# Kernel optimization log

Measured on AMD Instinct MI355X. Metric: run time of the kernel, lower is better.

## Reference

```python
import jax, jax.numpy as jnp
import numpy as np

B, S, D, H = 2, 2048, 1024, 16
DK = D // H


def setup_inputs() -> dict:
    key = jax.random.key(0)
    ks = jax.random.split(key, 6)
    inp = {
        "mha_input": jax.random.normal(ks[0], (B, S, D), dtype=jnp.float32),
        "mask": jax.random.randint(ks[1], (B, S), 0, 2, dtype=jnp.int32),
        "Wq_w": jax.random.normal(ks[2], (D, D), dtype=jnp.float32) * 0.02,
        "Wq_b": jnp.zeros((D,), dtype=jnp.float32),
        "Wk_w": jax.random.normal(ks[3], (D, D), dtype=jnp.float32) * 0.02,
        "Wk_b": jnp.zeros((D,), dtype=jnp.float32),
        "Wv_w": jax.random.normal(ks[4], (D, D), dtype=jnp.float32) * 0.02,
        "Wv_b": jnp.zeros((D,), dtype=jnp.float32),
        "Wo_w": jax.random.normal(ks[5], (D, D), dtype=jnp.float32) * 0.02,
        "Wo_b": jnp.zeros((D,), dtype=jnp.float32),
    }
    return inp


def _mha(x, mask, Wq_w, Wq_b, Wk_w, Wk_b, Wv_w, Wv_b, Wo_w, Wo_b):
    b, s, d = x.shape
    # nn.Linear: x @ W.T + b
    q = (x @ Wq_w.T + Wq_b).reshape(b, s, H, DK).transpose(0, 2, 1, 3)  # [B,H,S,DK]
    k = (x @ Wk_w.T + Wk_b).reshape(b, s, H, DK).transpose(0, 2, 1, 3)
    v = (x @ Wv_w.T + Wv_b).reshape(b, s, H, DK).transpose(0, 2, 1, 3)
    scores = jnp.einsum("bhqd,bhkd->bhqk", q, k) / jnp.sqrt(jnp.float32(DK))
    # prefix mask: key columns < count_nonzero(mask[i]) are kept, rest -inf
    lengths = jnp.count_nonzero(mask, axis=1)                # [B]
    valid = jnp.arange(s)[None, :] < lengths[:, None]        # [B,S]
    scores = jnp.where(valid[:, None, None, :], scores, -jnp.inf)
    attn = jax.nn.softmax(scores, axis=-1)
    out = jnp.einsum("bhqk,bhkd->bhqd", attn, v)             # [B,H,S,DK]
    concat = out.transpose(0, 2, 1, 3).reshape(b, s, d)      # [B,S,D]
    return concat @ Wo_w.T + Wo_b


def reference(mha_input, mask, Wq_w, Wq_b, Wk_w, Wk_b, Wv_w, Wv_b, Wo_w, Wo_b):
    return _mha(mha_input, mask, Wq_w, Wq_b, Wk_w, Wk_b, Wv_w, Wv_b, Wo_w, Wo_b)
```

## Files before the change

### kernel.cpp

```cpp
#include <hip/hip_runtime.h>

using bf16x8 = __attribute__((ext_vector_type(8))) short;
using f32x4  = __attribute__((ext_vector_type(4))) float;

#define S_LEN 2048
#define NHEAD 16
#define DKH   64
#define HSZ   (S_LEN * DKH * 32)
#define QSCALE 0.18033688011112042f

#if __has_builtin(__builtin_amdgcn_exp2f)
#define EXP2(x) __builtin_amdgcn_exp2f(x)
#else
#define EXP2(x) exp2f(x)
#endif

__device__ __forceinline__ unsigned short f2bf(float x) {
  unsigned u = __builtin_bit_cast(unsigned, x);
  u += 0x7FFFu + ((u >> 16) & 1u);
  return (unsigned short)(u >> 16);
}

__device__ __forceinline__ void gload_lds16(const void* g, void* l) {
  __builtin_amdgcn_global_load_lds(
      (const __attribute__((address_space(1))) unsigned int*)g,
      (__attribute__((address_space(3))) unsigned int*)l, 16, 0, 0);
}

__global__ void cvt_kernel(const float* __restrict__ src,
                           unsigned short* __restrict__ dst, int n4) {
  int i = blockIdx.x * blockDim.x + threadIdx.x;
  if (i < n4) {
    float4 v = ((const float4*)src)[i];
    ushort4 o;
    o.x = f2bf(v.x); o.y = f2bf(v.y); o.z = f2bf(v.z); o.w = f2bf(v.w);
    ((ushort4*)dst)[i] = o;
  }
}

__global__ void lens_kernel(const int* __restrict__ mask, int* __restrict__ lens) {
  __shared__ int sred[256];
  const int b = blockIdx.x;
  int c = 0;
  for (int s = threadIdx.x; s < S_LEN; s += 256) c += (mask[b * S_LEN + s] != 0) ? 1 : 0;
  sred[threadIdx.x] = c;
  __syncthreads();
  for (int st = 128; st > 0; st >>= 1) {
    if (threadIdx.x < st) sred[threadIdx.x] += sred[threadIdx.x + st];
    __syncthreads();
  }
  if (threadIdx.x == 0) lens[b] = sred[0];
}

template <int MODE>
__global__ __launch_bounds__(256) void gemm_kernel(
    const unsigned short* __restrict__ A, const unsigned short* __restrict__ B,
    const float* __restrict__ b0, const float* __restrict__ b1,
    const float* __restrict__ b2, unsigned short* __restrict__ outQKV,
    float* __restrict__ outF, const int K) {
  __shared__ __align__(16) unsigned short As[128 * 32];
  __shared__ __align__(16) unsigned short Bs[128 * 32];
  const int tid = threadIdx.x;
  const int w = tid >> 6, lane = tid & 63;
  const int wm = w >> 1, wn = w & 1;
  const int r = lane & 15, g = lane >> 4;
  const int tm = blockIdx.y * 128, tn = blockIdx.x * 128;

  f32x4 acc[4][4] = {};
  const char* Ab = (const char*)A;
  const char* Bb = (const char*)B;
  char* AsB = (char*)As;
  char* BsB = (char*)Bs;

  for (int k0 = 0; k0 < K; k0 += 32) {
#pragma unroll
    for (int i = 0; i < 2; ++i) {
      const int o = (w * 2 + i) * 1024 + lane * 16;
      const int row = o >> 6, colb = o & 63;
      gload_lds16(Ab + ((size_t)(tm + row) * K + k0) * 2 + colb, AsB + (w * 2 + i) * 1024);
      gload_lds16(Bb + ((size_t)(tn + row) * K + k0) * 2 + colb, BsB + (w * 2 + i) * 1024);
    }
    __syncthreads();
    bf16x8 af[4], bfr[4];
#pragma unroll
    for (int mi = 0; mi < 4; ++mi)
      af[mi] = *(const bf16x8*)(AsB + (wm * 64 + mi * 16 + r) * 64 + g * 16);
#pragma unroll
    for (int ni = 0; ni < 4; ++ni)
      bfr[ni] = *(const bf16x8*)(BsB + (wn * 64 + ni * 16 + r) * 64 + g * 16);
#pragma unroll
    for (int mi = 0; mi < 4; ++mi)
#pragma unroll
      for (int ni = 0; ni < 4; ++ni)
        acc[mi][ni] = __builtin_amdgcn_mfma_f32_16x16x32_bf16(af[mi], bfr[ni], acc[mi][ni], 0, 0, 0);
    __syncthreads();
  }

  if (MODE == 0) {
    const int mat = tn >> 10;
    const float* bp = (mat == 0) ? b0 : (mat == 1) ? b1 : b2;
    const float scale = (mat == 0) ? QSCALE : 1.0f;
    unsigned short* dst = outQKV + (size_t)mat * HSZ;
#pragma unroll
    for (int mi = 0; mi < 4; ++mi)
#pragma unroll
      for (int ni = 0; ni < 4; ++ni)
#pragma unroll
        for (int reg = 0; reg < 4; ++reg) {
          const int m = tm + wm * 64 + mi * 16 + 4 * g + reg;
          const int n = tn + wn * 64 + ni * 16 + r;
          const int nn = n & 1023;
          const float v = (acc[mi][ni][reg] + bp[nn]) * scale;
          const int bI = m >> 11, s = m & 2047, hh = nn >> 6, dk = nn & 63;
          if (mat == 2) {
            dst[(size_t)((bI * NHEAD + hh) * DKH + dk) * S_LEN + s] = f2bf(v);
          } else {
            dst[(size_t)((bI * NHEAD + hh) * S_LEN + s) * DKH + dk] = f2bf(v);
          }
        }
  } else {
#pragma unroll
    for (int mi = 0; mi < 4; ++mi)
#pragma unroll
      for (int ni = 0; ni < 4; ++ni)
#pragma unroll
        for (int reg = 0; reg < 4; ++reg) {
          const int m = tm + wm * 64 + mi * 16 + 4 * g + reg;
          const int n = tn + wn * 64 + ni * 16 + r;
          outF[(size_t)m * 1024 + n] = acc[mi][ni][reg] + b0[n];
        }
  }
}

__device__ __forceinline__ void online_sm(f32x4* st, float& mrun, float& lrun,
                                          f32x4* oacc, int g) {
  float mloc = st[0][0];
#pragma unroll
  for (int f = 0; f < 4; ++f)
#pragma unroll
    for (int q = 0; q < 4; ++q) mloc = fmaxf(mloc, st[f][q]);
  mloc = fmaxf(mloc, __shfl_xor(mloc, 16));
  mloc = fmaxf(mloc, __shfl_xor(mloc, 32));
  const float mnew = fmaxf(mrun, mloc);
  const float alpha = EXP2(mrun - mnew);
  mrun = mnew;
  float psum = 0.f;
#pragma unroll
  for (int f = 0; f < 4; ++f)
#pragma unroll
    for (int q = 0; q < 4; ++q) {
      const float p = EXP2(st[f][q] - mnew);
      st[f][q] = p;
      psum += p;
    }
  psum += __shfl_xor(psum, 16);
  psum += __shfl_xor(psum, 32);
  lrun = lrun * alpha + psum;
  float areg[4];
#pragma unroll
  for (int q = 0; q < 4; ++q) areg[q] = __shfl(alpha, 4 * g + q);
#pragma unroll
  for (int f = 0; f < 4; ++f)
#pragma unroll
    for (int q = 0; q < 4; ++q) oacc[f][q] *= areg[q];
}

__global__ __launch_bounds__(256) void attn_kernel(
    const unsigned short* __restrict__ qkv, const int* __restrict__ lens,
    unsigned short* __restrict__ outc) {
  __shared__ __align__(16) unsigned short Kt[2][4096];
  __shared__ __align__(16) unsigned short Vt[2][4096];
  __shared__ __align__(16) unsigned short Pl[4][2][1024];
  const int tid = threadIdx.x;
  const int w = tid >> 6, lane = tid & 63;
  const int r = lane & 15, g = lane >> 4;
  const int bh = blockIdx.y;
  const int b = bh >> 4, h = bh & 15;
  const int q0 = blockIdx.x * 128;

  const unsigned short* Qp = qkv;
  const unsigned short* Kp = qkv + HSZ;
  const unsigned short* VTp = qkv + 2 * (size_t)HSZ;

  const size_t qbase = (size_t)(bh * S_LEN + q0 + w * 32 + r) * DKH;
  const bf16x8 qa0 = *(const bf16x8*)(Qp + qbase + g * 8);
  const bf16x8 qa1 = *(const bf16x8*)(Qp + qbase + 32 + g * 8);
  const bf16x8 qb0 = *(const bf16x8*)(Qp + qbase + 16 * DKH + g * 8);
  const bf16x8 qb1 = *(const bf16x8*)(Qp + qbase + 16 * DKH + 32 + g * 8);

  const int L = lens[b];
  const int nt = (L + 63) >> 6;
  float mA = -__builtin_inff(), lA = 0.f;
  float mB = -__builtin_inff(), lB = 0.f;
  f32x4 oA[4] = {}, oB[4] = {};

  char* PA = (char*)Pl[w][0];
  char* PB = (char*)Pl[w][1];
  const int swp = (r & 7) << 4;

  const char* kgb0 = (const char*)(Kp + (size_t)bh * S_LEN * DKH);
  const char* vgb0 = (const char*)(VTp + (size_t)bh * DKH * S_LEN);

  auto stage = [&](int tt, int bb) {
    const char* kgb = kgb0 + (size_t)tt * 64 * DKH * 2;
    const char* vgb = vgb0 + (size_t)tt * 64 * 2;
    char* kd = (char*)Kt[bb];
    char* vd = (char*)Vt[bb];
#pragma unroll
    for (int i = 0; i < 2; ++i) {
      const int o = i * 4096 + w * 1024 + lane * 16;
      const int row = o >> 7, colb = o & 127;
      const int cs = colb ^ ((row & 7) << 4);
      gload_lds16(kgb + row * 128 + cs, kd + i * 4096 + w * 1024);
      gload_lds16(vgb + (size_t)row * (S_LEN * 2) + cs, vd + i * 4096 + w * 1024);
    }
  };

  if (nt > 0) stage(0, 0);
  __syncthreads();

  int buf = 0;
  for (int t = 0; t < nt; ++t) {
    if (t + 1 < nt) stage(t + 1, buf ^ 1);

    const char* KtB = (const char*)Kt[buf];
    f32x4 sa[4], sb[4];
    __builtin_amdgcn_s_setprio(1);
#pragma unroll
    for (int f = 0; f < 4; ++f) {
      const int c = f * 16 + r;
      const int sw = (c & 7) << 4;
      const bf16x8 k0 = *(const bf16x8*)(KtB + c * 128 + ((g * 16) ^ sw));
      const bf16x8 k1 = *(const bf16x8*)(KtB + c * 128 + ((64 + g * 16) ^ sw));
      f32x4 x = {};
      x = __builtin_amdgcn_mfma_f32_16x16x32_bf16(k0, qa0, x, 0, 0, 0);
      x = __builtin_amdgcn_mfma_f32_16x16x32_bf16(k1, qa1, x, 0, 0, 0);
      sa[f] = x;
      f32x4 y = {};
      y = __builtin_amdgcn_mfma_f32_16x16x32_bf16(k0, qb0, y, 0, 0, 0);
      y = __builtin_amdgcn_mfma_f32_16x16x32_bf16(k1, qb1, y, 0, 0, 0);
      sb[f] = y;
    }
    __builtin_amdgcn_s_setprio(0);

    const int kv0 = t * 64;
    if (t == nt - 1) {
#pragma unroll
      for (int f = 0; f < 4; ++f)
#pragma unroll
        for (int q = 0; q < 4; ++q)
          if (kv0 + f * 16 + 4 * g + q >= L) {
            sa[f][q] = -__builtin_inff();
            sb[f][q] = -__builtin_inff();
          }
    }

    online_sm(sa, mA, lA, oA, g);
    online_sm(sb, mB, lB, oB, g);

#pragma unroll
    for (int f = 0; f < 4; ++f) {
      ushort4 pw;
      pw.x = f2bf(sa[f][0]); pw.y = f2bf(sa[f][1]);
      pw.z = f2bf(sa[f][2]); pw.w = f2bf(sa[f][3]);
      *(ushort4*)(PA + r * 128 + ((f * 32 + g * 8) ^ swp)) = pw;
      ushort4 qw;
      qw.x = f2bf(sb[f][0]); qw.y = f2bf(sb[f][1]);
      qw.z = f2bf(sb[f][2]); qw.w = f2bf(sb[f][3]);
      *(ushort4*)(PB + r * 128 + ((f * 32 + g * 8) ^ swp)) = qw;
    }

    const char* VtB = (const char*)Vt[buf];
#pragma unroll
    for (int c2 = 0; c2 < 2; ++c2) {
      const bf16x8 pa = *(const bf16x8*)(PA + r * 128 + ((c2 * 64 + g * 16) ^ swp));
      const bf16x8 pb = *(const bf16x8*)(PB + r * 128 + ((c2 * 64 + g * 16) ^ swp));
      __builtin_amdgcn_s_setprio(1);
#pragma unroll
      for (int f = 0; f < 4; ++f) {
        const int dk = f * 16 + r;
        const bf16x8 vf =
            *(const bf16x8*)(VtB + dk * 128 + ((c2 * 64 + g * 16) ^ ((dk & 7) << 4)));
        oA[f] = __builtin_amdgcn_mfma_f32_16x16x32_bf16(pa, vf, oA[f], 0, 0, 0);
        oB[f] = __builtin_amdgcn_mfma_f32_16x16x32_bf16(pb, vf, oB[f], 0, 0, 0);
      }
      __builtin_amdgcn_s_setprio(0);
    }

    __syncthreads();
    buf ^= 1;
  }

  const float iA = 1.0f / lA;
  const float iB = 1.0f / lB;
  float rA[4], rB[4];
#pragma unroll
  for (int q = 0; q < 4; ++q) {
    rA[q] = __shfl(iA, 4 * g + q);
    rB[q] = __shfl(iB, 4 * g + q);
  }
#pragma unroll
  for (int f = 0; f < 4; ++f) {
    const int dk = f * 16 + r;
#pragma unroll
    for (int q = 0; q < 4; ++q) {
      const int rowA = q0 + w * 32 + 4 * g + q;
      outc[(size_t)(b * S_LEN + rowA) * 1024 + h * DKH + dk] = f2bf(oA[f][q] * rA[q]);
      const int rowB = rowA + 16;
      outc[(size_t)(b * S_LEN + rowB) * 1024 + h * DKH + dk] = f2bf(oB[f][q] * rB[q]);
    }
  }
}

extern "C" void kernel_launch(void* const* d_in, const int* in_sizes, int n_in,
                              void* d_out, int out_size, void* d_ws, size_t ws_size,
                              hipStream_t stream) {
  const float* x  = (const float*)d_in[0];
  const int* mask = (const int*)d_in[1];
  const float* wq = (const float*)d_in[2];
  const float* bq = (const float*)d_in[3];
  const float* wk = (const float*)d_in[4];
  const float* bk = (const float*)d_in[5];
  const float* wv = (const float*)d_in[6];
  const float* bv = (const float*)d_in[7];
  const float* wo = (const float*)d_in[8];
  const float* bo = (const float*)d_in[9];
  (void)in_sizes; (void)n_in; (void)out_size; (void)ws_size;

  char* ws = (char*)d_ws;
  unsigned short* xb  = (unsigned short*)ws;
  unsigned short* wb  = (unsigned short*)(ws + 8388608);
  unsigned short* wob = (unsigned short*)(ws + 14680064);
  unsigned short* qkv = (unsigned short*)(ws + 16777216);
  unsigned short* ao  = (unsigned short*)(ws + 41943040);
  int* lens           = (int*)(ws + 50331648);
  float* out          = (float*)d_out;

  cvt_kernel<<<4096, 256, 0, stream>>>(x, xb, 1048576);
  cvt_kernel<<<1024, 256, 0, stream>>>(wq, wb, 262144);
  cvt_kernel<<<1024, 256, 0, stream>>>(wk, wb + 1048576, 262144);
  cvt_kernel<<<1024, 256, 0, stream>>>(wv, wb + 2097152, 262144);
  cvt_kernel<<<1024, 256, 0, stream>>>(wo, wob, 262144);
  lens_kernel<<<2, 256, 0, stream>>>(mask, lens);

  gemm_kernel<0><<<dim3(24, 32), 256, 0, stream>>>(xb, wb, bq, bk, bv, qkv, nullptr, 1024);
  attn_kernel<<<dim3(16, 32), 256, 0, stream>>>(qkv, lens, ao);
  gemm_kernel<1><<<dim3(8, 32), 256, 0, stream>>>(ao, wob, bo, nullptr, nullptr, nullptr, out, 1024);
}
```

Measured before the change: 216.6 us.

## Double-buffer GEMM LDS tiles, vectorize epilogue stores, fuse conversion kernels

The GEMM kernel now keeps two LDS buffers so the next k-tile load is issued while the current one feeds the MFMAs, and it raises wave priority around the MFMA block. The MFMA operand order is swapped per output matrix so each lane holds contiguous output elements, which lets the epilogue write ushort4 or float4 vectors instead of scalar scattered stores. The five fp32-to-bf16 conversion launches are merged into one kernel. This doubles LDS use per block, which may lower occupancy, and adds branching in the conversion kernel.

```diff
diff --git a/kernel.cpp b/kernel.cpp
--- a/kernel.cpp
+++ b/kernel.cpp
@@ -15,6 +15,8 @@
 #define EXP2(x) exp2f(x)
 #endif
 
+template <bool B> struct BoolC { static constexpr bool value = B; };
+
 __device__ __forceinline__ unsigned short f2bf(float x) {
   unsigned u = __builtin_bit_cast(unsigned, x);
   u += 0x7FFFu + ((u >> 16) & 1u);
@@ -27,15 +29,36 @@
       (__attribute__((address_space(3))) unsigned int*)l, 16, 0, 0);
 }
 
-__global__ void cvt_kernel(const float* __restrict__ src,
-                           unsigned short* __restrict__ dst, int n4) {
-  int i = blockIdx.x * blockDim.x + threadIdx.x;
-  if (i < n4) {
-    float4 v = ((const float4*)src)[i];
-    ushort4 o;
-    o.x = f2bf(v.x); o.y = f2bf(v.y); o.z = f2bf(v.z); o.w = f2bf(v.w);
-    ((ushort4*)dst)[i] = o;
-  }
+__global__ void cvt_all_kernel(const float* __restrict__ x,
+                               const float* __restrict__ wq,
+                               const float* __restrict__ wk,
+                               const float* __restrict__ wv,
+                               const float* __restrict__ wo,
+                               unsigned short* __restrict__ xb,
+                               unsigned short* __restrict__ wb,
+                               unsigned short* __restrict__ wob) {
+  const int i = blockIdx.x * 256 + threadIdx.x;
+  const float* s;
+  unsigned short* d;
+  if (i < 1048576) {
+    s = x + (size_t)i * 4;            d = xb + (size_t)i * 4;
+  } else if (i < 1310720) {
+    const int j = i - 1048576;
+    s = wq + (size_t)j * 4;           d = wb + (size_t)j * 4;
+  } else if (i < 1572864) {
+    const int j = i - 1310720;
+    s = wk + (size_t)j * 4;           d = wb + 1048576 + (size_t)j * 4;
+  } else if (i < 1835008) {
+    const int j = i - 1572864;
+    s = wv + (size_t)j * 4;           d = wb + 2097152 + (size_t)j * 4;
+  } else {
+    const int j = i - 1835008;
+    s = wo + (size_t)j * 4;           d = wob + (size_t)j * 4;
+  }
+  float4 v = *(const float4*)s;
+  ushort4 o;
+  o.x = f2bf(v.x); o.y = f2bf(v.y); o.z = f2bf(v.z); o.w = f2bf(v.w);
+  *(ushort4*)d = o;
 }
 
 __global__ void lens_kernel(const int* __restrict__ mask, int* __restrict__ lens) {
@@ -58,77 +81,128 @@
     const float* __restrict__ b0, const float* __restrict__ b1,
     const float* __restrict__ b2, unsigned short* __restrict__ outQKV,
     float* __restrict__ outF, const int K) {
-  __shared__ __align__(16) unsigned short As[128 * 32];
-  __shared__ __align__(16) unsigned short Bs[128 * 32];
+  __shared__ __align__(16) unsigned short As[2][128 * 32];
+  __shared__ __align__(16) unsigned short Bs[2][128 * 32];
   const int tid = threadIdx.x;
   const int w = tid >> 6, lane = tid & 63;
   const int wm = w >> 1, wn = w & 1;
   const int r = lane & 15, g = lane >> 4;
   const int tm = blockIdx.y * 128, tn = blockIdx.x * 128;
+  const int mat = (MODE == 0) ? (tn >> 10) : 0;
 
   f32x4 acc[4][4] = {};
   const char* Ab = (const char*)A;
   const char* Bb = (const char*)B;
-  char* AsB = (char*)As;
-  char* BsB = (char*)Bs;
-
-  for (int k0 = 0; k0 < K; k0 += 32) {
+  const int nk = K >> 5;
+
+  auto stage = [&](int kt, int bb) {
+    char* ad = (char*)As[bb];
+    char* bd = (char*)Bs[bb];
+    const int k0 = kt * 32;
 #pragma unroll
     for (int i = 0; i < 2; ++i) {
       const int o = (w * 2 + i) * 1024 + lane * 16;
       const int row = o >> 6, colb = o & 63;
-      gload_lds16(Ab + ((size_t)(tm + row) * K + k0) * 2 + colb, AsB + (w * 2 + i) * 1024);
-      gload_lds16(Bb + ((size_t)(tn + row) * K + k0) * 2 + colb, BsB + (w * 2 + i) * 1024);
-    }
+      gload_lds16(Ab + ((size_t)(tm + row) * K + k0) * 2 + colb, ad + (w * 2 + i) * 1024);
+      gload_lds16(Bb + ((size_t)(tn + row) * K + k0) * 2 + colb, bd + (w * 2 + i) * 1024);
+    }
+  };
+
+  auto kloop = [&](auto swap_c) {
+    constexpr bool SW = decltype(swap_c)::value;
+    stage(0, 0);
     __syncthreads();
-    bf16x8 af[4], bfr[4];
-#pragma unroll
-    for (int mi = 0; mi < 4; ++mi)
-      af[mi] = *(const bf16x8*)(AsB + (wm * 64 + mi * 16 + r) * 64 + g * 16);
-#pragma unroll
-    for (int ni = 0; ni < 4; ++ni)
-      bfr[ni] = *(const bf16x8*)(BsB + (wn * 64 + ni * 16 + r) * 64 + g * 16);
-#pragma unroll
-    for (int mi = 0; mi < 4; ++mi)
+    int buf = 0;
+    for (int kt = 0; kt < nk; ++kt) {
+      if (kt + 1 < nk) stage(kt + 1, buf ^ 1);
+      const char* AsB = (const char*)As[buf];
+      const char* BsB = (const char*)Bs[buf];
+      bf16x8 af[4], bfr[4];
+#pragma unroll
+      for (int mi = 0; mi < 4; ++mi)
+        af[mi] = *(const bf16x8*)(AsB + (wm * 64 + mi * 16 + r) * 64 + g * 16);
 #pragma unroll
       for (int ni = 0; ni < 4; ++ni)
-        acc[mi][ni] = __builtin_amdgcn_mfma_f32_16x16x32_bf16(af[mi], bfr[ni], acc[mi][ni], 0, 0, 0);
-    __syncthreads();
-  }
+        bfr[ni] = *(const bf16x8*)(BsB + (wn * 64 + ni * 16 + r) * 64 + g * 16);
+      __builtin_amdgcn_s_setprio(1);
+#pragma unroll
+      for (int mi = 0; mi < 4; ++mi)
+#pragma unroll
+        for (int ni = 0; ni < 4; ++ni) {
+          if constexpr (SW)
+            acc[mi][ni] = __builtin_amdgcn_mfma_f32_16x16x32_bf16(bfr[ni], af[mi], acc[mi][ni], 0, 0, 0);
+          else
+            acc[mi][ni] = __builtin_amdgcn_mfma_f32_16x16x32_bf16(af[mi], bfr[ni], acc[mi][ni], 0, 0, 0);
+        }
+      __builtin_amdgcn_s_setprio(0);
+      __syncthreads();
+      buf ^= 1;
+    }
+  };
+
+  if (MODE == 1 || mat != 2) kloop(BoolC<true>{});
+  else                        kloop(BoolC<false>{});
 
   if (MODE == 0) {
-    const int mat = tn >> 10;
-    const float* bp = (mat == 0) ? b0 : (mat == 1) ? b1 : b2;
-    const float scale = (mat == 0) ? QSCALE : 1.0f;
-    unsigned short* dst = outQKV + (size_t)mat * HSZ;
-#pragma unroll
-    for (int mi = 0; mi < 4; ++mi)
-#pragma unroll
-      for (int ni = 0; ni < 4; ++ni)
-#pragma unroll
-        for (int reg = 0; reg < 4; ++reg) {
-          const int m = tm + wm * 64 + mi * 16 + 4 * g + reg;
-          const int n = tn + wn * 64 + ni * 16 + r;
-          const int nn = n & 1023;
-          const float v = (acc[mi][ni][reg] + bp[nn]) * scale;
-          const int bI = m >> 11, s = m & 2047, hh = nn >> 6, dk = nn & 63;
-          if (mat == 2) {
-            dst[(size_t)((bI * NHEAD + hh) * DKH + dk) * S_LEN + s] = f2bf(v);
-          } else {
-            dst[(size_t)((bI * NHEAD + hh) * S_LEN + s) * DKH + dk] = f2bf(v);
-          }
+    if (mat != 2) {
+      const float* bp = mat ? b1 : b0;
+      const float scale = mat ? 1.0f : QSCALE;
+      unsigned short* dst = outQKV + (size_t)mat * HSZ;
+      const int tnl = tn & 1023;
+#pragma unroll
+      for (int ni = 0; ni < 4; ++ni) {
+        const int nb = tnl + wn * 64 + ni * 16 + 4 * g;
+        const float4 b4 = *(const float4*)(bp + nb);
+        const int hh = nb >> 6, dkb = nb & 63;
+#pragma unroll
+        for (int mi = 0; mi < 4; ++mi) {
+          const int m = tm + wm * 64 + mi * 16 + r;
+          const int bI = m >> 11, s = m & 2047;
+          ushort4 pw;
+          pw.x = f2bf((acc[mi][ni][0] + b4.x) * scale);
+          pw.y = f2bf((acc[mi][ni][1] + b4.y) * scale);
+          pw.z = f2bf((acc[mi][ni][2] + b4.z) * scale);
+          pw.w = f2bf((acc[mi][ni][3] + b4.w) * scale);
+          *(ushort4*)(dst + (size_t)((bI * NHEAD + hh) * S_LEN + s) * DKH + dkb) = pw;
         }
+      }
+    } else {
+      unsigned short* dst = outQKV + 2 * (size_t)HSZ;
+      const int tnl = tn & 1023;
+#pragma unroll
+      for (int ni = 0; ni < 4; ++ni) {
+        const int n = tnl + wn * 64 + ni * 16 + r;
+        const float bias = b2[n];
+        const int hh = n >> 6, dk = n & 63;
+#pragma unroll
+        for (int mi = 0; mi < 4; ++mi) {
+          const int m = tm + wm * 64 + mi * 16 + 4 * g;
+          const int bI = m >> 11, s0 = m & 2047;
+          ushort4 pw;
+          pw.x = f2bf(acc[mi][ni][0] + bias);
+          pw.y = f2bf(acc[mi][ni][1] + bias);
+          pw.z = f2bf(acc[mi][ni][2] + bias);
+          pw.w = f2bf(acc[mi][ni][3] + bias);
+          *(ushort4*)(dst + (size_t)((bI * NHEAD + hh) * DKH + dk) * S_LEN + s0) = pw;
+        }
+      }
+    }
   } else {
 #pragma unroll
-    for (int mi = 0; mi < 4; ++mi)
-#pragma unroll
-      for (int ni = 0; ni < 4; ++ni)
-#pragma unroll
-        for (int reg = 0; reg < 4; ++reg) {
-          const int m = tm + wm * 64 + mi * 16 + 4 * g + reg;
-          const int n = tn + wn * 64 + ni * 16 + r;
-          outF[(size_t)m * 1024 + n] = acc[mi][ni][reg] + b0[n];
-        }
+    for (int ni = 0; ni < 4; ++ni) {
+      const int nb = tn + wn * 64 + ni * 16 + 4 * g;
+      const float4 b4 = *(const float4*)(b0 + nb);
+#pragma unroll
+      for (int mi = 0; mi < 4; ++mi) {
+        const int m = tm + wm * 64 + mi * 16 + r;
+        float4 o4;
+        o4.x = acc[mi][ni][0] + b4.x;
+        o4.y = acc[mi][ni][1] + b4.y;
+        o4.z = acc[mi][ni][2] + b4.z;
+        o4.w = acc[mi][ni][3] + b4.w;
+        *(float4*)(outF + (size_t)m * 1024 + nb) = o4;
+      }
+    }
   }
 }
 
@@ -336,11 +410,7 @@
   int* lens           = (int*)(ws + 50331648);
   float* out          = (float*)d_out;
 
-  cvt_kernel<<<4096, 256, 0, stream>>>(x, xb, 1048576);
-  cvt_kernel<<<1024, 256, 0, stream>>>(wq, wb, 262144);
-  cvt_kernel<<<1024, 256, 0, stream>>>(wk, wb + 1048576, 262144);
-  cvt_kernel<<<1024, 256, 0, stream>>>(wv, wb + 2097152, 262144);
-  cvt_kernel<<<1024, 256, 0, stream>>>(wo, wob, 262144);
+  cvt_all_kernel<<<8192, 256, 0, stream>>>(x, wq, wk, wv, wo, xb, wb, wob);
   lens_kernel<<<2, 256, 0, stream>>>(mask, lens);
 
   gemm_kernel<0><<<dim3(24, 32), 256, 0, stream>>>(xb, wb, bq, bk, bv, qkv, nullptr, 1024);
```

Result: faster. 211.7 us (-2.3%).
